# Optimization experiments

Hardware: AMD Instinct MI355X
Metric: run time of the kernel (lower is better)

## Reference

```python
import jax, jax.numpy as jnp
import numpy as np

V, E, SH, H = 10004, 300, 1024, 512
B, T = 128, 50
PAD = 10003


def setup_inputs() -> dict:
    key = jax.random.key(0)
    ks = jax.random.split(key, 13)
    s = 0.05
    emb = s * jax.random.normal(ks[0], (V, E), dtype=jnp.float32)
    emb = emb.at[PAD].set(0.0)  # padding_idx row is zero
    G = 2 * H  # GRU hidden size is 2*hid_size
    Wih = s * jax.random.normal(ks[1], (3 * G, E), dtype=jnp.float32)
    Whh = s * jax.random.normal(ks[2], (3 * G, G), dtype=jnp.float32)
    bih = s * jax.random.normal(ks[3], (3 * G,), dtype=jnp.float32)
    bhh = s * jax.random.normal(ks[4], (3 * G,), dtype=jnp.float32)
    W1 = s * jax.random.normal(ks[5], (H, SH), dtype=jnp.float32)
    b1 = s * jax.random.normal(ks[6], (H,), dtype=jnp.float32)
    W2 = s * jax.random.normal(ks[7], (E, G), dtype=jnp.float32)
    b2 = s * jax.random.normal(ks[8], (E,), dtype=jnp.float32)
    Wout = s * jax.random.normal(ks[9], (V, E), dtype=jnp.float32)
    ses_encoding = jax.random.normal(ks[10], (1, B, SH), dtype=jnp.float32)
    x = jax.random.randint(ks[11], (B, T), 0, 10000)
    return {"ses_encoding": ses_encoding, "x": x, "emb": emb, "Wih": Wih,
            "Whh": Whh, "bih": bih, "bhh": bhh, "W1": W1, "b1": b1,
            "W2": W2, "b2": b2, "Wout": Wout}


def reference(ses_encoding, x, emb, Wih, Whh, bih, bhh, W1, b1, W2, b2, Wout):
    hid = W1.shape[0]            # hid_size
    G = Whh.shape[1]             # 2*hid_size (GRU hidden)
    # ses_encoding = tanh(lin1(ses_encoding)), then viewed to [1, B, hid]
    ses = jnp.tanh(jnp.einsum('lbs,hs->lbh', ses_encoding, W1) + b1)[0]  # [B, hid]
    emb_all = emb[x]             # [B, T, E] (dropout inactive at eval)

    def step(h, e_t):
        # GRU hidden input each step: concat(prev_half, ses) -> [B, 2*hid]
        Hfull = jnp.concatenate([h, ses], axis=-1)
        gx = e_t @ Wih.T + bih                      # [B, 3G]
        gh = Hfull @ Whh.T + bhh                    # [B, 3G]
        r = jax.nn.sigmoid(gx[:, :G] + gh[:, :G])
        z = jax.nn.sigmoid(gx[:, G:2 * G] + gh[:, G:2 * G])
        n = jnp.tanh(gx[:, 2 * G:] + r * gh[:, 2 * G:])
        hnew = (1.0 - z) * n + z * Hfull            # [B, 2*hid]
        o = hnew @ W2.T + b2 + e_t                  # lin2(hid_o) + residual emb
        logits = o @ Wout.T                         # [B, V]
        return hnew[:, :hid], logits

    _, logits = jax.lax.scan(step, ses, jnp.swapaxes(emb_all, 0, 1))
    return jnp.swapaxes(logits, 0, 1)               # [B, T, V]
```

## Files before the change

kernel.cpp:

```cpp
#include <hip/hip_runtime.h>


typedef __bf16 bf16x8 __attribute__((ext_vector_type(8)));
typedef float f32x4 __attribute__((ext_vector_type(4)));
typedef unsigned long long u64;

__global__ void cvt_kernel(const float* __restrict__ src, int srows, int scols,
                           int sstride, int soff,
                           __bf16* __restrict__ dst, int drows, int dcols) {
    int idx = blockIdx.x * 256 + threadIdx.x;
    int total = drows * dcols;
    if (idx >= total) return;
    int r = idx / dcols, c = idx % dcols;
    float v = 0.0f;
    if (r < srows && c < scols) v = src[(size_t)r * sstride + soff + c];
    dst[idx] = (__bf16)v;
}

__global__ void emb_kernel(const int* __restrict__ x, const float* __restrict__ emb,
                           __bf16* __restrict__ embbf) {
    int m = blockIdx.x;
    int t = m >> 7, b = m & 127;
    int tok = x[b * 50 + t];
    const float* src = emb + (size_t)tok * 300;
    for (int i = threadIdx.x; i < 320; i += 64) {
        float v = (i < 300) ? src[i] : 0.0f;
        embbf[(size_t)m * 320 + i] = (__bf16)v;
    }
}

struct GemmParams {
    const __bf16* A; int lda;
    const __bf16* B; int ldb; int Brows;
    int K;
    const float* bias;
    float* outF; int ldo; int Nstore;
    __bf16* outBf;
    const __bf16* res;
    const float* add2;
    int ld2; int add2lim;
};

template <int EPI>
__launch_bounds__(256, 2)
__global__ void gemm_bt(GemmParams p) {
    __shared__ __bf16 As[128][40];
    __shared__ __bf16 Bs[128][40];

    const int tid = threadIdx.x;
    const int lane = tid & 63;
    const int wid = tid >> 6;
    const int wr = wid >> 1, wc = wid & 1;
    const int m0 = blockIdx.x * 128, c0 = blockIdx.y * 128;
    const int lrow = lane & 15;
    const int kq = lane >> 4;

    f32x4 acc[4][4];
#pragma unroll
    for (int i = 0; i < 4; ++i)
#pragma unroll
        for (int j = 0; j < 4; ++j) acc[i][j] = (f32x4){0.f, 0.f, 0.f, 0.f};

    for (int kb = 0; kb < p.K; kb += 32) {
#pragma unroll
        for (int i = 0; i < 2; ++i) {
            int chunk = i * 256 + tid;
            int row = chunk >> 2;
            int cc = (chunk & 3) * 8;
            bf16x8 va = *reinterpret_cast<const bf16x8*>(
                p.A + (size_t)(m0 + row) * p.lda + kb + cc);
            *reinterpret_cast<bf16x8*>(&As[row][cc]) = va;
            bf16x8 vb;
#pragma unroll
            for (int q = 0; q < 8; ++q) vb[q] = (__bf16)0.0f;
            int grow = c0 + row;
            if (grow < p.Brows)
                vb = *reinterpret_cast<const bf16x8*>(
                    p.B + (size_t)grow * p.ldb + kb + cc);
            *reinterpret_cast<bf16x8*>(&Bs[row][cc]) = vb;
        }
        __syncthreads();

        bf16x8 af[4], bfr[4];
#pragma unroll
        for (int m = 0; m < 4; ++m)
            af[m] = *reinterpret_cast<const bf16x8*>(&As[wr * 64 + m * 16 + lrow][kq * 8]);
#pragma unroll
        for (int n = 0; n < 4; ++n)
            bfr[n] = *reinterpret_cast<const bf16x8*>(&Bs[wc * 64 + n * 16 + lrow][kq * 8]);
#pragma unroll
        for (int m = 0; m < 4; ++m)
#pragma unroll
            for (int n = 0; n < 4; ++n)
                acc[m][n] = __builtin_amdgcn_mfma_f32_16x16x32_bf16(
                    af[m], bfr[n], acc[m][n], 0, 0, 0);
        __syncthreads();
    }

#pragma unroll
    for (int m = 0; m < 4; ++m) {
#pragma unroll
        for (int n = 0; n < 4; ++n) {
#pragma unroll
            for (int i = 0; i < 4; ++i) {
                int r = m0 + wr * 64 + m * 16 + kq * 4 + i;
                int c = c0 + wc * 64 + n * 16 + lrow;
                float v = acc[m][n][i];
                if constexpr (EPI == 1) {
                    v = tanhf(v + p.bias[c]);
                    p.outBf[(size_t)r * p.ldo + c] = (__bf16)v;
                    p.outF[(size_t)c * 128 + r] = v;
                } else if constexpr (EPI == 2) {
                    int ro = (r & 127) * 50 + (r >> 7);
                    if (c < 300) {
                        v += p.bias[c] + (float)p.res[(size_t)r * 320 + c];
                        p.outBf[(size_t)ro * 320 + c] = (__bf16)v;
                    } else if (c < 320) {
                        p.outBf[(size_t)ro * 320 + c] = (__bf16)0.0f;
                    }
                } else if constexpr (EPI == 3) {
                    if (c < p.Nstore) p.outF[(size_t)r * p.ldo + c] = v;
                } else {
                    if (c < p.Brows) {
                        float v2 = v + p.bias[r];
                        if (p.add2 && r < p.add2lim)
                            v2 += p.add2[(size_t)r * 128 + (c & 127)];
                        p.outF[(size_t)(c >> 7) * p.ldo + (size_t)r * 128 + (c & 127)] = v2;
                    }
                }
            }
        }
    }
}

#define SCAN_NB 64
__launch_bounds__(256, 1)
__global__ void scan_kernel(const __bf16* __restrict__ Whh_a,
                            const float* __restrict__ gxT,
                            const float* __restrict__ ghcT,
                            const float* __restrict__ sesT,
                            u64* __restrict__ F,
                            unsigned* __restrict__ cnt) {
    __shared__ char smem[131072];
    char* Ws = smem;
    char* Hs = smem + 98304;
    const int tid = threadIdx.x;
    const int lane = tid & 63;
    const int wid = tid >> 6;
    const int wr = wid >> 1, wc = wid & 1;
    const int bid = blockIdx.x;
    const int q = bid >> 4;
    const int j0 = (bid & 15) * 32;
    const int lrow = lane & 15, kq = lane >> 4;

    for (int it = 0; it < 24; ++it) {
        int c = it * 256 + tid;
        int rl = c >> 6, o16 = c & 63;
        int g = rl >> 5, jj = rl & 31;
        bf16x8 v = *reinterpret_cast<const bf16x8*>(
            Whh_a + (size_t)(g * 1024 + j0 + jj) * 512 + o16 * 8);
        *reinterpret_cast<bf16x8*>(Ws + rl * 1024 + ((o16 * 16) ^ ((rl & 7) << 4))) = v;
    }

    const int b_g = q * 32 + wc * 16 + lrow;
    const int jbase = j0 + wr * 16 + kq * 4;

    float cn[4], hprev[4], gcur[12], gpre[12];
#pragma unroll
    for (int i = 0; i < 4; ++i) {
        cn[i] = ghcT[(size_t)(2048 + jbase + i) * 128 + b_g];
        hprev[i] = sesT[(size_t)(jbase + i) * 128 + b_g];
    }
#pragma unroll
    for (int i = 0; i < 4; ++i) {
        gpre[i]     = gxT[(size_t)(jbase + i) * 128 + b_g];
        gpre[4 + i] = gxT[(size_t)(1024 + jbase + i) * 128 + b_g];
        gpre[8 + i] = gxT[(size_t)(2048 + jbase + i) * 128 + b_g];
    }

    for (int t = 0; t < 50; ++t) {
        for (int it = 0; it < 16; ++it) {
            int c = it * 256 + tid;
            int rl = c >> 7, o8 = c & 127;
            u64 v = __hip_atomic_load(
                F + ((size_t)t * 128 + q * 32 + rl) * 256 + o8,
                __ATOMIC_RELAXED, __HIP_MEMORY_SCOPE_AGENT);
            *reinterpret_cast<u64*>(Hs + rl * 1024 + ((o8 * 8) ^ ((rl & 7) << 4))) = v;
        }
#pragma unroll
        for (int i = 0; i < 12; ++i) gcur[i] = gpre[i];
        {
            int tn = (t < 49) ? t + 1 : 49;
            const float* gxt = gxT + (size_t)tn * 3072 * 128;
#pragma unroll
            for (int i = 0; i < 4; ++i) {
                gpre[i]     = gxt[(size_t)(jbase + i) * 128 + b_g];
                gpre[4 + i] = gxt[(size_t)(1024 + jbase + i) * 128 + b_g];
                gpre[8 + i] = gxt[(size_t)(2048 + jbase + i) * 128 + b_g];
            }
        }
        __syncthreads();

        f32x4 acc[3];
#pragma unroll
        for (int g = 0; g < 3; ++g) acc[g] = (f32x4){0.f, 0.f, 0.f, 0.f};
        const int hrow = wc * 16 + lrow;
        const int arow0 = wr * 16 + lrow;
        for (int kb = 0; kb < 16; ++kb) {
            int ko = kb * 64 + kq * 16;
            bf16x8 hfrag = *reinterpret_cast<const bf16x8*>(
                Hs + hrow * 1024 + (ko ^ ((hrow & 7) << 4)));
#pragma unroll
            for (int g = 0; g < 3; ++g) {
                int arow = g * 32 + arow0;
                bf16x8 wfrag = *reinterpret_cast<const bf16x8*>(
                    Ws + arow * 1024 + (ko ^ ((arow & 7) << 4)));
                acc[g] = __builtin_amdgcn_mfma_f32_16x16x32_bf16(
                    wfrag, hfrag, acc[g], 0, 0, 0);
            }
        }

        union { u64 u; __bf16 h[4]; } pk;
#pragma unroll
        for (int i = 0; i < 4; ++i) {
            float r = 1.0f / (1.0f + expf(-(gcur[i] + acc[0][i])));
            float z = 1.0f / (1.0f + expf(-(gcur[4 + i] + acc[1][i])));
            float nn = tanhf(gcur[8 + i] + r * (acc[2][i] + cn[i]));
            float hn = (1.0f - z) * nn + z * hprev[i];
            hprev[i] = hn;
            pk.h[i] = (__bf16)hn;
        }
        __hip_atomic_store(
            F + ((size_t)(t + 1) * 128 + b_g) * 256 + (jbase >> 2), pk.u,
            __ATOMIC_RELAXED, __HIP_MEMORY_SCOPE_AGENT);

        if (t < 49) {
            __syncthreads();
            if (tid == 0) {
                __hip_atomic_fetch_add(cnt + q * 32, 1u,
                                       __ATOMIC_RELAXED, __HIP_MEMORY_SCOPE_AGENT);
                unsigned tgt = (unsigned)(t + 1) * 16u;
                while (__hip_atomic_load(cnt + q * 32, __ATOMIC_RELAXED,
                                         __HIP_MEMORY_SCOPE_AGENT) < tgt)
                    __builtin_amdgcn_s_sleep(1);
            }
            __syncthreads();
        }
    }
}

__launch_bounds__(256, 1)
__global__ void tail_kernel(const __bf16* __restrict__ Whh_a,
                            const float* __restrict__ gxT,
                            const float* __restrict__ ghcT,
                            const float* __restrict__ sesT,
                            __bf16* __restrict__ F) {
    __shared__ char smem[131072];
    char* Ws = smem;
    char* Hs = smem + 98304;
    const int tid = threadIdx.x;
    const int lane = tid & 63;
    const int wid = tid >> 6;
    const int wr = wid >> 1, wc = wid & 1;
    const int bid = blockIdx.x;
    const int tg = bid >> 6;
    const int rem = bid & 63;
    const int q = rem >> 4;
    const int j0 = 512 + (rem & 15) * 32;
    const int lrow = lane & 15, kq = lane >> 4;

    for (int it = 0; it < 24; ++it) {
        int c = it * 256 + tid;
        int rl = c >> 6, o16 = c & 63;
        int g = rl >> 5, jj = rl & 31;
        bf16x8 v = *reinterpret_cast<const bf16x8*>(
            Whh_a + (size_t)(g * 1024 + j0 + jj) * 512 + o16 * 8);
        *reinterpret_cast<bf16x8*>(Ws + rl * 1024 + ((o16 * 16) ^ ((rl & 7) << 4))) = v;
    }

    const int b_g = q * 32 + wc * 16 + lrow;
    const int jbase = j0 + wr * 16 + kq * 4;

    float cn[4], sv[4];
#pragma unroll
    for (int i = 0; i < 4; ++i) {
        cn[i] = ghcT[(size_t)(2048 + jbase + i) * 128 + b_g];
        sv[i] = sesT[(size_t)(jbase + i - 512) * 128 + b_g];
    }

    for (int tt = tg * 10; tt < tg * 10 + 10; ++tt) {
        for (int it = 0; it < 8; ++it) {
            int c = it * 256 + tid;
            int rl = c >> 6, o16 = c & 63;
            bf16x8 v = *reinterpret_cast<const bf16x8*>(
                F + ((size_t)tt * 128 + q * 32 + rl) * 1024 + o16 * 8);
            *reinterpret_cast<bf16x8*>(Hs + rl * 1024 + ((o16 * 16) ^ ((rl & 7) << 4))) = v;
        }
        const float* gxt = gxT + (size_t)tt * 3072 * 128;
        float g0[12];
#pragma unroll
        for (int i = 0; i < 4; ++i) {
            g0[i]     = gxt[(size_t)(jbase + i) * 128 + b_g];
            g0[4 + i] = gxt[(size_t)(1024 + jbase + i) * 128 + b_g];
            g0[8 + i] = gxt[(size_t)(2048 + jbase + i) * 128 + b_g];
        }
        __syncthreads();

        f32x4 acc[3];
#pragma unroll
        for (int g = 0; g < 3; ++g) acc[g] = (f32x4){0.f, 0.f, 0.f, 0.f};
        const int hrow = wc * 16 + lrow;
        const int arow0 = wr * 16 + lrow;
        for (int kb = 0; kb < 16; ++kb) {
            int ko = kb * 64 + kq * 16;
            bf16x8 hfrag = *reinterpret_cast<const bf16x8*>(
                Hs + hrow * 1024 + (ko ^ ((hrow & 7) << 4)));
#pragma unroll
            for (int g = 0; g < 3; ++g) {
                int arow = g * 32 + arow0;
                bf16x8 wfrag = *reinterpret_cast<const bf16x8*>(
                    Ws + arow * 1024 + (ko ^ ((arow & 7) << 4)));
                acc[g] = __builtin_amdgcn_mfma_f32_16x16x32_bf16(
                    wfrag, hfrag, acc[g], 0, 0, 0);
            }
        }

        union { u64 u; __bf16 h[4]; } pk;
#pragma unroll
        for (int i = 0; i < 4; ++i) {
            float r = 1.0f / (1.0f + expf(-(g0[i] + acc[0][i])));
            float z = 1.0f / (1.0f + expf(-(g0[4 + i] + acc[1][i])));
            float nn = tanhf(g0[8 + i] + r * (acc[2][i] + cn[i]));
            pk.h[i] = (__bf16)((1.0f - z) * nn + z * sv[i]);
        }
        *reinterpret_cast<u64*>(F + ((size_t)(tt + 1) * 128 + b_g) * 1024 + jbase) = pk.u;
        __syncthreads();
    }
}

extern "C" void kernel_launch(void* const* d_in, const int* in_sizes, int n_in,
                              void* d_out, int out_size, void* d_ws, size_t ws_size,
                              hipStream_t stream) {
    const float* ses_enc = (const float*)d_in[0];
    const int*   x       = (const int*)d_in[1];
    const float* emb     = (const float*)d_in[2];
    const float* Wih     = (const float*)d_in[3];
    const float* Whh     = (const float*)d_in[4];
    const float* bih     = (const float*)d_in[5];
    const float* bhh     = (const float*)d_in[6];
    const float* W1      = (const float*)d_in[7];
    const float* b1      = (const float*)d_in[8];
    const float* W2      = (const float*)d_in[9];
    const float* b2      = (const float*)d_in[10];
    const float* Wout    = (const float*)d_in[11];
    float* out = (float*)d_out;

    char* ws = (char*)d_ws;
    float*  sesT      = (float*)(ws + 0);
    float*  ghcT      = (float*)(ws + 262144);
    __bf16* o_bf      = (__bf16*)(ws + 1835008);
    __bf16* W1_bf     = (__bf16*)(ws + 5931008);
    __bf16* Whh_a_bf  = (__bf16*)(ws + 6979584);
    __bf16* Whh_b_bf  = (__bf16*)(ws + 10125312);
    __bf16* Wih_bf    = (__bf16*)(ws + 13271040);
    __bf16* W2_bf     = (__bf16*)(ws + 15237120);
    __bf16* Wout_bf   = (__bf16*)(ws + 15851520);
    __bf16* sesenc_bf = (__bf16*)(ws + 22323200);
    unsigned* cnt     = (unsigned*)(ws + 22585344);

    char* ob = (char*)d_out;
    float*  gxT     = (float*)ob;
    __bf16* emb_bf  = (__bf16*)(ob + 80000000);
    __bf16* F       = (__bf16*)(ob + 88000000);

    dim3 blk(256);
    auto cvt = [&](const float* src, int sr, int sc, int ss, int so,
                   __bf16* dst, int dr, int dc) {
        int total = dr * dc;
        cvt_kernel<<<(total + 255) / 256, 256, 0, stream>>>(src, sr, sc, ss, so, dst, dr, dc);
    };
    cvt(W1,      512, 1024, 1024, 0,   W1_bf,     512, 1024);
    cvt(Whh,    3072,  512, 1024, 0,   Whh_a_bf, 3072,  512);
    cvt(Whh,    3072,  512, 1024, 512, Whh_b_bf, 3072,  512);
    cvt(Wih,    3072,  300,  300, 0,   Wih_bf,   3072,  320);
    cvt(W2,      300, 1024, 1024, 0,   W2_bf,     300, 1024);
    cvt(Wout,  10004,  300,  300, 0,   Wout_bf, 10112,  320);
    cvt(ses_enc, 128, 1024, 1024, 0,   sesenc_bf, 128, 1024);
    emb_kernel<<<6400, 64, 0, stream>>>(x, emb, emb_bf);
    hipMemsetAsync(cnt, 0, 1024, stream);

    GemmParams P;

    P = {sesenc_bf, 1024, W1_bf, 1024, 512, 1024, b1, sesT, 1024, 512, F,
         nullptr, nullptr, 0, 0};
    gemm_bt<1><<<dim3(1, 4), blk, 0, stream>>>(P);

    P = {Whh_b_bf, 512, F, 1024, 128, 512, bhh, ghcT, 0, 0, nullptr,
         nullptr, nullptr, 0, 0};
    gemm_bt<4><<<dim3(24, 1), blk, 0, stream>>>(P);

    P = {Wih_bf, 320, emb_bf, 320, 6400, 320, bih, gxT, 3072 * 128, 0, nullptr,
         nullptr, ghcT, 0, 2048};
    gemm_bt<4><<<dim3(24, 50), blk, 0, stream>>>(P);

    scan_kernel<<<SCAN_NB, 256, 0, stream>>>(
        Whh_a_bf, gxT, ghcT, sesT, (u64*)F, cnt);

    tail_kernel<<<320, 256, 0, stream>>>(Whh_a_bf, gxT, ghcT, sesT, F);

    P = {F + 128 * 1024, 1024, W2_bf, 1024, 300, 1024, b2, nullptr, 0, 300, o_bf,
         emb_bf, nullptr, 0, 0};
    gemm_bt<2><<<dim3(50, 3), blk, 0, stream>>>(P);

    P = {o_bf, 320, Wout_bf, 320, 10112, 320, nullptr, out, 10004, 10004, nullptr,
         nullptr, nullptr, 0, 0};
    gemm_bt<3><<<dim3(50, 79), blk, 0, stream>>>(P);

    (void)in_sizes; (void)n_in; (void)out_size; (void)ws_size;
}
```

Measured before the change: 708.8 us.

## Replace scan counter barrier with sentinel-flagged dataflow polling on hidden state

The per-step group barrier (atomic counter plus two __syncthreads) in the recurrent scan is removed. Instead, the hidden-state buffer is prefilled with a NaN sentinel pattern, and each wave polls its own MFMA operand fragments straight from global memory until none equal the sentinel. The LDS staging of H goes away with it. This is meant to cut the latency of the step-to-step barrier on the serial critical path. In exchange it adds a prefill kernel, redundant global loads per wave, and relies on a computed bf16 value never matching the sentinel pattern.

```diff
diff --git a/kernel.cpp b/kernel.cpp
--- a/kernel.cpp
+++ b/kernel.cpp
@@ -4,6 +4,8 @@
 typedef __bf16 bf16x8 __attribute__((ext_vector_type(8)));
 typedef float f32x4 __attribute__((ext_vector_type(4)));
 typedef unsigned long long u64;
+
+#define SENT 0xFFC1FFC1FFC1FFC1ull
 
 __global__ void cvt_kernel(const float* __restrict__ src, int srows, int scols,
                            int sstride, int soff,
@@ -27,6 +29,13 @@
         float v = (i < 300) ? src[i] : 0.0f;
         embbf[(size_t)m * 320 + i] = (__bf16)v;
     }
+}
+
+__global__ void prefill_kernel(u64* __restrict__ F) {
+    size_t idx = (size_t)blockIdx.x * 256 + threadIdx.x;
+    size_t row = idx >> 7, off = idx & 127;
+    __hip_atomic_store(F + (128 + row) * 256 + off, SENT,
+                       __ATOMIC_RELAXED, __HIP_MEMORY_SCOPE_AGENT);
 }
 
 struct GemmParams {
@@ -139,11 +148,8 @@
                             const float* __restrict__ gxT,
                             const float* __restrict__ ghcT,
                             const float* __restrict__ sesT,
-                            u64* __restrict__ F,
-                            unsigned* __restrict__ cnt) {
-    __shared__ char smem[131072];
-    char* Ws = smem;
-    char* Hs = smem + 98304;
+                            u64* __restrict__ F) {
+    __shared__ char Ws[98304];
     const int tid = threadIdx.x;
     const int lane = tid & 63;
     const int wid = tid >> 6;
@@ -178,15 +184,9 @@
         gpre[8 + i] = gxT[(size_t)(2048 + jbase + i) * 128 + b_g];
     }
 
+    __syncthreads();
+
     for (int t = 0; t < 50; ++t) {
-        for (int it = 0; it < 16; ++it) {
-            int c = it * 256 + tid;
-            int rl = c >> 7, o8 = c & 127;
-            u64 v = __hip_atomic_load(
-                F + ((size_t)t * 128 + q * 32 + rl) * 256 + o8,
-                __ATOMIC_RELAXED, __HIP_MEMORY_SCOPE_AGENT);
-            *reinterpret_cast<u64*>(Hs + rl * 1024 + ((o8 * 8) ^ ((rl & 7) << 4))) = v;
-        }
 #pragma unroll
         for (int i = 0; i < 12; ++i) gcur[i] = gpre[i];
         {
@@ -199,24 +199,42 @@
                 gpre[8 + i] = gxt[(size_t)(2048 + jbase + i) * 128 + b_g];
             }
         }
-        __syncthreads();
+
+        const u64* rowp = F + ((size_t)t * 128 + b_g) * 256 + kq * 2;
+        u64 hv[32];
+        for (;;) {
+            bool ok = true;
+#pragma unroll
+            for (int kb = 0; kb < 16; ++kb) {
+                u64 a = __hip_atomic_load(rowp + kb * 8,
+                                          __ATOMIC_RELAXED, __HIP_MEMORY_SCOPE_AGENT);
+                u64 b = __hip_atomic_load(rowp + kb * 8 + 1,
+                                          __ATOMIC_RELAXED, __HIP_MEMORY_SCOPE_AGENT);
+                hv[2 * kb] = a;
+                hv[2 * kb + 1] = b;
+                ok &= (a != SENT) & (b != SENT);
+            }
+            if (__all(ok)) break;
+            __builtin_amdgcn_s_sleep(1);
+        }
 
         f32x4 acc[3];
 #pragma unroll
         for (int g = 0; g < 3; ++g) acc[g] = (f32x4){0.f, 0.f, 0.f, 0.f};
-        const int hrow = wc * 16 + lrow;
         const int arow0 = wr * 16 + lrow;
+#pragma unroll
         for (int kb = 0; kb < 16; ++kb) {
+            union { u64 u[2]; bf16x8 v; } hf;
+            hf.u[0] = hv[2 * kb];
+            hf.u[1] = hv[2 * kb + 1];
             int ko = kb * 64 + kq * 16;
-            bf16x8 hfrag = *reinterpret_cast<const bf16x8*>(
-                Hs + hrow * 1024 + (ko ^ ((hrow & 7) << 4)));
 #pragma unroll
             for (int g = 0; g < 3; ++g) {
                 int arow = g * 32 + arow0;
                 bf16x8 wfrag = *reinterpret_cast<const bf16x8*>(
                     Ws + arow * 1024 + (ko ^ ((arow & 7) << 4)));
                 acc[g] = __builtin_amdgcn_mfma_f32_16x16x32_bf16(
-                    wfrag, hfrag, acc[g], 0, 0, 0);
+                    wfrag, hf.v, acc[g], 0, 0, 0);
             }
         }
 
@@ -233,19 +251,6 @@
         __hip_atomic_store(
             F + ((size_t)(t + 1) * 128 + b_g) * 256 + (jbase >> 2), pk.u,
             __ATOMIC_RELAXED, __HIP_MEMORY_SCOPE_AGENT);
-
-        if (t < 49) {
-            __syncthreads();
-            if (tid == 0) {
-                __hip_atomic_fetch_add(cnt + q * 32, 1u,
-                                       __ATOMIC_RELAXED, __HIP_MEMORY_SCOPE_AGENT);
-                unsigned tgt = (unsigned)(t + 1) * 16u;
-                while (__hip_atomic_load(cnt + q * 32, __ATOMIC_RELAXED,
-                                         __HIP_MEMORY_SCOPE_AGENT) < tgt)
-                    __builtin_amdgcn_s_sleep(1);
-            }
-            __syncthreads();
-        }
     }
 }
 
@@ -366,7 +371,6 @@
     __bf16* W2_bf     = (__bf16*)(ws + 15237120);
     __bf16* Wout_bf   = (__bf16*)(ws + 15851520);
     __bf16* sesenc_bf = (__bf16*)(ws + 22323200);
-    unsigned* cnt     = (unsigned*)(ws + 22585344);
 
     char* ob = (char*)d_out;
     float*  gxT     = (float*)ob;
@@ -387,7 +391,7 @@
     cvt(Wout,  10004,  300,  300, 0,   Wout_bf, 10112,  320);
     cvt(ses_enc, 128, 1024, 1024, 0,   sesenc_bf, 128, 1024);
     emb_kernel<<<6400, 64, 0, stream>>>(x, emb, emb_bf);
-    hipMemsetAsync(cnt, 0, 1024, stream);
+    prefill_kernel<<<3200, 256, 0, stream>>>((u64*)F);
 
     GemmParams P;
 
@@ -404,7 +408,7 @@
     gemm_bt<4><<<dim3(24, 50), blk, 0, stream>>>(P);
 
     scan_kernel<<<SCAN_NB, 256, 0, stream>>>(
-        Whh_a_bf, gxT, ghcT, sesT, (u64*)F, cnt);
+        Whh_a_bf, gxT, ghcT, sesT, (u64*)F);
 
     tail_kernel<<<320, 256, 0, stream>>>(Whh_a_bf, gxT, ghcT, sesT, F);
 
```

Measured after the change: 753.1 us. +6.2%, slower.
